# Performance work log

Measured on AMD Instinct MI355X. Metric: run time of the kernel, lower is better.

The kernel has to match this reference:

```python
import jax, jax.numpy as jnp
import numpy as np

DIM = 192
HEADS = 6
HIDDEN = 384  # int(DIM * 2.0)


def _ln(x, w, b):
    # WithBias LayerNorm over channel dim (torch normalizes last dim of b,(hw),c)
    mu = jnp.mean(x, axis=1, keepdims=True)
    var = jnp.var(x, axis=1, keepdims=True)
    return (x - mu) / jnp.sqrt(var + 1e-5) * w[None, :, None, None] + b[None, :, None, None]


def _conv1x1(x, w):  # w: [O, I, 1, 1]
    return jnp.einsum('bihw,oi->bohw', x, w[:, :, 0, 0])


def _dwconv3(x, w):  # depthwise 3x3, w: [C, 1, 3, 3]
    return jax.lax.conv_general_dilated(
        x, w, window_strides=(1, 1), padding=((1, 1), (1, 1)),
        feature_group_count=x.shape[1],
        dimension_numbers=('NCHW', 'OIHW', 'NCHW'))


def _l2norm(x):  # F.normalize along last axis
    n = jnp.sqrt(jnp.sum(x * x, axis=-1, keepdims=True))
    return x / jnp.maximum(n, 1e-12)


def setup_inputs() -> dict:
    key = jax.random.key(0)
    ks = jax.random.split(key, 16)
    s = 0.02
    d = {}
    d['x'] = jax.random.normal(ks[0], (2, DIM, 128, 128), dtype=jnp.float32)
    d['k_v'] = jax.random.normal(ks[1], (2, 256), dtype=jnp.float32)
    d['ln1_w'] = jnp.ones((DIM,), jnp.float32)
    d['ln1_b'] = jnp.zeros((DIM,), jnp.float32)
    d['temp'] = jnp.ones((HEADS, 1, 1), jnp.float32)
    d['w_kR'] = jax.random.normal(ks[2], (DIM * 3 // 4, 192), jnp.float32) * s
    d['w_kI'] = jax.random.normal(ks[3], (DIM // 4, 64), jnp.float32) * s
    d['w_qR'] = jax.random.normal(ks[4], (DIM, DIM * 3 // 4, 1, 1), jnp.float32) * s
    d['w_qdw'] = jax.random.normal(ks[5], (DIM, 1, 3, 3), jnp.float32) * s
    d['w_kvI'] = jax.random.normal(ks[6], (DIM * 2, DIM // 4, 1, 1), jnp.float32) * s
    d['w_kvdw'] = jax.random.normal(ks[7], (DIM * 2, 1, 3, 3), jnp.float32) * s
    d['w_po'] = jax.random.normal(ks[8], (DIM, DIM, 1, 1), jnp.float32) * s
    d['ln2_w'] = jnp.ones((DIM,), jnp.float32)
    d['ln2_b'] = jnp.zeros((DIM,), jnp.float32)
    d['w_ffk'] = jax.random.normal(ks[9], (DIM, 256), jnp.float32) * s
    d['w_pin'] = jax.random.normal(ks[10], (HIDDEN * 2, DIM, 1, 1), jnp.float32) * s
    d['w_dw'] = jax.random.normal(ks[11], (HIDDEN * 2, 1, 3, 3), jnp.float32) * s
    d['w_pout'] = jax.random.normal(ks[12], (DIM, HIDDEN, 1, 1), jnp.float32) * s
    return d


def reference(x, k_v, ln1_w, ln1_b, temp, w_kR, w_kI, w_qR, w_qdw, w_kvI, w_kvdw,
              w_po, ln2_w, ln2_b, w_ffk, w_pin, w_dw, w_pout):
    b, c, h, w = x.shape
    c3 = c * 3 // 4
    # ---- Rttention on norm1(x) ----
    xn = _ln(x, ln1_w, ln1_b)
    kvr = (k_v[:, :192] @ w_kR.T)[:, :, None, None]   # [b, 3c/4, 1, 1]
    kvi = (k_v[:, 192:] @ w_kI.T)[:, :, None, None]   # [b, c/4, 1, 1]
    x_r = xn[:, :c3] * kvr + xn[:, :c3]
    x_i = xn[:, c3:] * kvi + xn[:, c3:]
    q = _dwconv3(_conv1x1(x_r, w_qR), w_qdw)          # [b, c, h, w]
    kv = _dwconv3(_conv1x1(x_i, w_kvI), w_kvdw)       # [b, 2c, h, w]
    k, v = jnp.split(kv, 2, axis=1)
    rh = lambda t: t.reshape(b, HEADS, c // HEADS, h * w)
    q = _l2norm(rh(q))
    k = _l2norm(rh(k))
    v = rh(v)
    # channel-wise attention: [b, head, c_h, c_h]
    attn = jax.nn.softmax(jnp.einsum('bhcd,bhed->bhce', q, k) * temp[None], axis=-1)
    out = jnp.einsum('bhce,bhed->bhcd', attn, v).reshape(b, c, h, w)
    x = x + _conv1x1(out, w_po)
    # ---- GDFN FeedForward on norm2(x) ----
    xn2 = _ln(x, ln2_w, ln2_b)
    kvf = (k_v @ w_ffk.T)[:, :, None, None]           # [b, c, 1, 1]
    y = xn2 * kvf + xn2
    y = _dwconv3(_conv1x1(y, w_pin), w_dw)            # [b, 2*hidden, h, w]
    y1, y2 = jnp.split(y, 2, axis=1)
    y = jax.nn.gelu(y1, approximate=False) * y2
    x = x + _conv1x1(y, w_pout)
    return (x, k_v)
```

## Files before the change

### kernel.cpp

```cpp
#include <hip/hip_runtime.h>
#include <math.h>

#define HW 16384
#define CDIM 192
#define C3 144
#define C4 48
#define NB 2
#define NPX 32768
#define HEADS 6

typedef unsigned short u16;
typedef unsigned int u32;
typedef __attribute__((ext_vector_type(8))) short bf16x8;
typedef __attribute__((ext_vector_type(4))) float f32x4;

__device__ __forceinline__ float bf2f(u16 u) {
    return __uint_as_float(((unsigned int)u) << 16);
}
__device__ __forceinline__ u16 f2bf(float f) {
    unsigned int x = __float_as_uint(f);
    unsigned int r = x + 0x7fffu + ((x >> 16) & 1u);
    return (u16)(r >> 16);
}

static inline float* wsf(void* ws, size_t off) { return (float*)((char*)ws + off); }
static inline u16* wsh(void* ws, size_t off) { return (u16*)((char*)ws + off); }

__global__ void k_setup(const float* __restrict__ kvv, const float* __restrict__ wkR,
                        const float* __restrict__ wkI, const float* __restrict__ wffk,
                        const float* __restrict__ wqR, const float* __restrict__ wkvI,
                        const float* __restrict__ wpo, const float* __restrict__ wpin,
                        const float* __restrict__ wpout,
                        const float* __restrict__ ln2w, const float* __restrict__ ln2b,
                        u16* __restrict__ wb, float* __restrict__ sm,
                        float* __restrict__ A2, float* __restrict__ B2,
                        float* __restrict__ tail) {
    int t = blockIdx.x * 256 + threadIdx.x;
    if (t < 313344) {
        float v;
        if (t < 30720) {
            int o = t / 160, i = t % 160;
            v = (i < 144) ? wqR[o * 144 + i] : 0.f;
        } else if (t < 55296) {
            int r = t - 30720; int o = r / 64, i = r % 64;
            v = (i < 48) ? wkvI[o * 48 + i] : 0.f;
        } else if (t < 92160) {
            v = wpo[t - 55296];
        } else if (t < 239616) {
            v = wpin[t - 92160];
        } else {
            v = wpout[t - 239616];
        }
        wb[t] = f2bf(v);
    } else if (t < 314112) {
        int r = t - 313344;
        if (r < 288) {
            int b = r / 144, o = r % 144;
            const float* v = kvv + b * 256;
            const float* w = wkR + o * 192;
            float s = 0.f;
            for (int j = 0; j < 192; j++) s += v[j] * w[j];
            sm[r] = s + 1.0f;
        } else if (r < 384) {
            int r2 = r - 288;
            int b = r2 / 48, o = r2 % 48;
            const float* v = kvv + b * 256 + 192;
            const float* w = wkI + o * 64;
            float s = 0.f;
            for (int j = 0; j < 64; j++) s += v[j] * w[j];
            sm[288 + r2] = s + 1.0f;
        } else {
            int r2 = r - 384;
            int b = r2 / 192, o = r2 % 192;
            const float* v = kvv + b * 256;
            const float* w = wffk + o * 256;
            float s = 0.f;
            for (int j = 0; j < 256; j++) s += v[j] * w[j];
            float sc = s + 1.0f;
            sm[384 + r2] = sc;
            A2[r2] = ln2w[o] * sc;
            B2[r2] = ln2b[o] * sc;
        }
    } else if (t < 314624) {
        int r = t - 314112;
        tail[r] = kvv[r];
    }
}

__global__ __launch_bounds__(256) void k_ln1(
    const float* __restrict__ xin,
    const float* __restrict__ lnw, const float* __restrict__ lnb,
    const float* __restrict__ sca, const float* __restrict__ scb,
    u16* __restrict__ outA, u16* __restrict__ outB) {
    __shared__ float red[2][16][16][4];
    __shared__ float mu_s[16][4], rstd_s[16][4];
    int t = threadIdx.x;
    int px4 = t & 15, cg = t >> 4;
    int base = blockIdx.x * 64;
    int b = base >> 14;
    int p = (base & 16383) + px4 * 4;
    float vals[12][4];
    float s[4] = {0.f, 0.f, 0.f, 0.f}, s2[4] = {0.f, 0.f, 0.f, 0.f};
#pragma unroll
    for (int j = 0; j < 12; j++) {
        int c = cg * 12 + j;
        size_t off = ((size_t)(b * CDIM + c)) * HW + p;
        float4 f = *(const float4*)(xin + off);
        float v[4] = {f.x, f.y, f.z, f.w};
#pragma unroll
        for (int q = 0; q < 4; q++) {
            vals[j][q] = v[q]; s[q] += v[q]; s2[q] += v[q] * v[q];
        }
    }
#pragma unroll
    for (int q = 0; q < 4; q++) { red[0][cg][px4][q] = s[q]; red[1][cg][px4][q] = s2[q]; }
    __syncthreads();
    if (t < 16) {
        float S[4] = {0.f, 0.f, 0.f, 0.f}, S2[4] = {0.f, 0.f, 0.f, 0.f};
        for (int g2 = 0; g2 < 16; g2++)
#pragma unroll
            for (int q = 0; q < 4; q++) { S[q] += red[0][g2][t][q]; S2[q] += red[1][g2][t][q]; }
#pragma unroll
        for (int q = 0; q < 4; q++) {
            float mu = S[q] * (1.0f / CDIM);
            float var = S2[q] * (1.0f / CDIM) - mu * mu;
            mu_s[t][q] = mu;
            rstd_s[t][q] = rsqrtf(var + 1e-5f);
        }
    }
    __syncthreads();
    float mu[4], rs[4];
#pragma unroll
    for (int q = 0; q < 4; q++) { mu[q] = mu_s[px4][q]; rs[q] = rstd_s[px4][q]; }
    float Ac[12], Bc[12];
#pragma unroll
    for (int j = 0; j < 12; j++) {
        int c = cg * 12 + j;
        float sc = (c < C3) ? sca[b * C3 + c] : scb[b * C4 + (c - C3)];
        Ac[j] = lnw[c] * sc;
        Bc[j] = lnb[c] * sc;
    }
    int isR = (cg < 12);
    size_t row0 = (size_t)b * HW + p;
    u16* basep = isR ? (outA + row0 * 160 + cg * 12)
                     : (outB + row0 * 64 + (cg * 12 - 144));
    int rowlen = isR ? 160 : 64;
#pragma unroll
    for (int q = 0; q < 4; q++) {
        u16 tmp[12];
#pragma unroll
        for (int j = 0; j < 12; j++)
            tmp[j] = f2bf((vals[j][q] - mu[q]) * rs[q] * Ac[j] + Bc[j]);
        u16* op = basep + q * rowlen;
        ushort4 o0 = {tmp[0], tmp[1], tmp[2], tmp[3]};
        ushort4 o1 = {tmp[4], tmp[5], tmp[6], tmp[7]};
        ushort4 o2 = {tmp[8], tmp[9], tmp[10], tmp[11]};
        *(ushort4*)(op) = o0;
        *(ushort4*)(op + 4) = o1;
        *(ushort4*)(op + 8) = o2;
    }
    if (cg == 0) {
        int4 z = {0, 0, 0, 0};
#pragma unroll
        for (int q = 0; q < 4; q++) {
            u16* pr = outA + (row0 + q) * 160 + 144;
            *(int4*)(pr) = z; *(int4*)(pr + 8) = z;
            u16* pi = outB + (row0 + q) * 64 + 48;
            *(int4*)(pi) = z; *(int4*)(pi + 8) = z;
        }
    }
}

template <int NCH, int MLOOP, int MODE>
__global__ __launch_bounds__(256, 2) void k_gemm_t(
    const u16* __restrict__ X, const u16* __restrict__ Wb,
    const void* __restrict__ resid, void* __restrict__ outp, int CO) {
    constexpr int CIP = NCH * 32;
    const int tid = threadIdx.x;
    const int n0 = blockIdx.x * 128;
    const int b = blockIdx.z;
    const int wave = tid >> 6, lane = tid & 63;
    const int quad = lane >> 4, l16 = lane & 15;
    const u16* brow = X + ((size_t)b * HW + n0 + wave * 32 + l16) * CIP + quad * 8;
    bf16x8 Bf[NCH][2];
#pragma unroll
    for (int ch = 0; ch < NCH; ch++) {
        Bf[ch][0] = *(const bf16x8*)(brow + ch * 32);
        Bf[ch][1] = *(const bf16x8*)(brow + 16 * CIP + ch * 32);
    }
#pragma unroll
    for (int ml = 0; ml < MLOOP; ml++) {
        const int m0 = (blockIdx.y * MLOOP + ml) * 64;
        const u16* arow = Wb + (size_t)(m0 + l16) * CIP + quad * 8;
        f32x4 acc[4][2] = {};
#pragma unroll
        for (int ch = 0; ch < NCH; ch++) {
            bf16x8 af[4];
#pragma unroll
            for (int mi = 0; mi < 4; mi++)
                af[mi] = *(const bf16x8*)(arow + mi * 16 * CIP + ch * 32);
#pragma unroll
            for (int mi = 0; mi < 4; mi++) {
                acc[mi][0] = __builtin_amdgcn_mfma_f32_16x16x32_bf16(af[mi], Bf[ch][0], acc[mi][0], 0, 0, 0);
                acc[mi][1] = __builtin_amdgcn_mfma_f32_16x16x32_bf16(af[mi], Bf[ch][1], acc[mi][1], 0, 0, 0);
            }
        }
#pragma unroll
        for (int mi = 0; mi < 4; mi++) {
#pragma unroll
            for (int ni = 0; ni < 2; ni++) {
                int c0 = m0 + mi * 16 + quad * 4;
                int px = n0 + wave * 32 + ni * 16 + l16;
                if (MODE == 0) {
                    u16* ob = (u16*)outp + ((size_t)b * CO + c0) * HW + px;
#pragma unroll
                    for (int r = 0; r < 4; r++) ob[(size_t)r * HW] = f2bf(acc[mi][ni][r]);
                } else {
                    const float* rp = (const float*)resid + ((size_t)b * 192 + c0) * HW + px;
                    ushort4 o;
                    o.x = f2bf(acc[mi][ni][0] + rp[0]);
                    o.y = f2bf(acc[mi][ni][1] + rp[(size_t)HW]);
                    o.z = f2bf(acc[mi][ni][2] + rp[(size_t)2 * HW]);
                    o.w = f2bf(acc[mi][ni][3] + rp[(size_t)3 * HW]);
                    *(ushort4*)((u16*)outp + ((size_t)b * HW + px) * 192 + c0) = o;
                }
            }
        }
    }
}

__global__ __launch_bounds__(256) void k_gemm_s(
    const u16* __restrict__ X, const u16* __restrict__ Wb,
    const u16* __restrict__ residT, float* __restrict__ outp) {
    constexpr int NCH = 12;
    constexpr int CIP = NCH * 32;
    __shared__ __align__(16) u16 Ws[64 * 32];
    __shared__ __align__(16) u16 Xs[32 * 130];
    const int tid = threadIdx.x;
    const int n0 = blockIdx.x * 128;
    const int m0 = blockIdx.y * 64;
    const int b = blockIdx.z;
    const u16* Xb = X + (size_t)b * 384 * HW + n0;
    const int wave = tid >> 6, lane = tid & 63;
    const int quad = lane >> 4, l16 = lane & 15;
    const int smr = tid >> 2, sk4 = tid & 3;
    const int skr = tid >> 3, sc0 = (tid & 7) * 16;
    f32x4 acc[4][2] = {};
    for (int ch = 0; ch < NCH; ch++) {
        const int k0 = ch * 32;
        if (ch) __syncthreads();
        {
            const int4 wv = *(const int4*)(Wb + (size_t)(m0 + smr) * CIP + k0 + sk4 * 8);
            *(int4*)&Ws[(smr << 5) + (((sk4 ^ (smr & 3)) & 3) << 3)] = wv;
        }
        {
            const u16* xc = Xb + (size_t)(k0 + skr) * HW + sc0;
            int4 r0 = *(const int4*)xc;
            int4 r1 = *(const int4*)(xc + 8);
            u32* dst = (u32*)&Xs[skr * 130 + sc0];
#pragma unroll
            for (int i = 0; i < 4; i++) dst[i] = ((const u32*)&r0)[i];
#pragma unroll
            for (int i = 0; i < 4; i++) dst[4 + i] = ((const u32*)&r1)[i];
        }
        __syncthreads();
        bf16x8 af[4];
#pragma unroll
        for (int mi = 0; mi < 4; mi++) {
            int row = mi * 16 + l16;
            af[mi] = *(const bf16x8*)&Ws[(row << 5) + ((quad ^ (row & 3)) << 3)];
        }
#pragma unroll
        for (int ni = 0; ni < 2; ni++) {
            int n = wave * 32 + ni * 16 + l16;
            bf16x8 bfr;
#pragma unroll
            for (int j = 0; j < 8; j++) bfr[j] = (short)Xs[(quad * 8 + j) * 130 + n];
#pragma unroll
            for (int mi = 0; mi < 4; mi++)
                acc[mi][ni] = __builtin_amdgcn_mfma_f32_16x16x32_bf16(af[mi], bfr, acc[mi][ni], 0, 0, 0);
        }
    }
#pragma unroll
    for (int mi = 0; mi < 4; mi++) {
#pragma unroll
        for (int ni = 0; ni < 2; ni++) {
            int c0 = m0 + mi * 16 + quad * 4;
            int px = n0 + wave * 32 + ni * 16 + l16;
            ushort4 rv = *(const ushort4*)(residT + ((size_t)b * HW + px) * 192 + c0);
            float* ob = outp + ((size_t)b * 192 + c0) * HW + px;
            ob[0] = acc[mi][ni][0] + bf2f(rv.x);
            ob[(size_t)HW] = acc[mi][ni][1] + bf2f(rv.y);
            ob[(size_t)2 * HW] = acc[mi][ni][2] + bf2f(rv.z);
            ob[(size_t)3 * HW] = acc[mi][ni][3] + bf2f(rv.w);
        }
    }
}

__global__ __launch_bounds__(256) void k_dw2(const u16* __restrict__ X,
                                             const float* __restrict__ Wd,
                                             u16* __restrict__ out, int C, int sqCh,
                                             float* __restrict__ sqp) {
    __shared__ float In[34 * 132];
    __shared__ float red[4];
    int bc = blockIdx.x >> 2, rt = blockIdx.x & 3;
    int b = bc / C, ch = bc % C;
    const u16* xb = X + (size_t)bc * HW;
    int t = threadIdx.x;
    int c0 = (t & 7) * 16;
    for (int r = t >> 3; r < 34; r += 32) {
        int y = rt * 32 - 1 + r;
        float* dst = &In[r * 132 + 1 + c0];
        if ((unsigned)y < 128u) {
            const u16* src = xb + y * 128 + c0;
            int4 r0 = *(const int4*)src;
            int4 r1 = *(const int4*)(src + 8);
            const u16* p0 = (const u16*)&r0;
            const u16* p1 = (const u16*)&r1;
#pragma unroll
            for (int i = 0; i < 8; i++) dst[i] = bf2f(p0[i]);
#pragma unroll
            for (int i = 0; i < 8; i++) dst[8 + i] = bf2f(p1[i]);
        } else {
#pragma unroll
            for (int i = 0; i < 16; i++) dst[i] = 0.f;
        }
    }
    if (t < 34) { In[t * 132] = 0.f; In[t * 132 + 129] = 0.f; }
    __syncthreads();
    const float* w = Wd + ch * 9;
    float w00 = w[0], w01 = w[1], w02 = w[2], w10 = w[3], w11 = w[4],
          w12 = w[5], w20 = w[6], w21 = w[7], w22 = w[8];
    int x = t & 127, rg = t >> 7;
    int base = rg * 16;
    float A2 = 0.f, A1 = 0.f, B1 = 0.f, ssq = 0.f;
    u16* ob = out + (size_t)bc * HW + (rt * 32 + base) * 128 + x;
#pragma unroll
    for (int r = 0; r < 18; r++) {
        const float* row = &In[(base + r) * 132 + x];
        float v0 = row[0], v1 = row[1], v2 = row[2];
        float h0 = w00 * v0 + w01 * v1 + w02 * v2;
        float h1 = w10 * v0 + w11 * v1 + w12 * v2;
        float h2 = w20 * v0 + w21 * v1 + w22 * v2;
        if (r >= 2) {
            float val = A2 + B1 + h2;
            ob[(size_t)(r - 2) * 128] = f2bf(val);
            ssq += val * val;
        }
        A2 = A1; A1 = h0; B1 = h1;
    }
    if (ch < sqCh) {
        for (int o = 32; o > 0; o >>= 1) ssq += __shfl_down(ssq, o, 64);
        int wid = t >> 6, lane = t & 63;
        if (lane == 0) red[wid] = ssq;
        __syncthreads();
        if (t == 0) sqp[((b * 192 + ch) << 2) | rt] = red[0] + red[1] + red[2] + red[3];
    }
}

__global__ __launch_bounds__(256) void k_dw_gelu2(const u16* __restrict__ G0,
                                                  const float* __restrict__ Wd,
                                                  u16* __restrict__ out) {
    __shared__ float In[2 * 34 * 132];
    int bc = blockIdx.x >> 2, rt = blockIdx.x & 3;
    int b = bc / 384, j = bc % 384;
    int t = threadIdx.x;
    int c0 = (t & 7) * 16;
    for (int pl = 0; pl < 2; pl++) {
        const u16* xb = G0 + ((size_t)b * 768 + pl * 384 + j) * HW;
        float* pla = &In[pl * 34 * 132];
        for (int r = t >> 3; r < 34; r += 32) {
            int y = rt * 32 - 1 + r;
            float* dst = &pla[r * 132 + 1 + c0];
            if ((unsigned)y < 128u) {
                const u16* src = xb + y * 128 + c0;
                int4 r0 = *(const int4*)src;
                int4 r1 = *(const int4*)(src + 8);
                const u16* p0 = (const u16*)&r0;
                const u16* p1 = (const u16*)&r1;
#pragma unroll
                for (int i = 0; i < 8; i++) dst[i] = bf2f(p0[i]);
#pragma unroll
                for (int i = 0; i < 8; i++) dst[8 + i] = bf2f(p1[i]);
            } else {
#pragma unroll
                for (int i = 0; i < 16; i++) dst[i] = 0.f;
            }
        }
        if (t < 34) { pla[t * 132] = 0.f; pla[t * 132 + 129] = 0.f; }
    }
    __syncthreads();
    const float* w1 = Wd + j * 9;
    const float* w2 = Wd + (384 + j) * 9;
    float a00 = w1[0], a01 = w1[1], a02 = w1[2], a10 = w1[3], a11 = w1[4],
          a12 = w1[5], a20 = w1[6], a21 = w1[7], a22 = w1[8];
    float b00 = w2[0], b01 = w2[1], b02 = w2[2], b10 = w2[3], b11 = w2[4],
          b12 = w2[5], b20 = w2[6], b21 = w2[7], b22 = w2[8];
    int x = t & 127, rg = t >> 7;
    int base = rg * 16;
    float A2a = 0.f, A1a = 0.f, B1a = 0.f;
    float A2b = 0.f, A1b = 0.f, B1b = 0.f;
    u16* ob = out + ((size_t)b * 384 + j) * HW + (rt * 32 + base) * 128 + x;
#pragma unroll
    for (int r = 0; r < 18; r++) {
        const float* r1p = &In[(base + r) * 132 + x];
        const float* r2p = r1p + 34 * 132;
        float u0 = r1p[0], u1 = r1p[1], u2 = r1p[2];
        float v0 = r2p[0], v1 = r2p[1], v2 = r2p[2];
        float h0a = a00 * u0 + a01 * u1 + a02 * u2;
        float h1a = a10 * u0 + a11 * u1 + a12 * u2;
        float h2a = a20 * u0 + a21 * u1 + a22 * u2;
        float h0b = b00 * v0 + b01 * v1 + b02 * v2;
        float h1b = b10 * v0 + b11 * v1 + b12 * v2;
        float h2b = b20 * v0 + b21 * v1 + b22 * v2;
        if (r >= 2) {
            float s1 = A2a + B1a + h2a;
            float s2 = A2b + B1b + h2b;
            float g = 0.5f * s1 * (1.0f + erff(s1 * 0.70710678118654752f));
            ob[(size_t)(r - 2) * 128] = f2bf(g * s2);
        }
        A2a = A1a; A1a = h0a; B1a = h1a;
        A2b = A1b; A1b = h0b; B1b = h1b;
    }
}

__global__ __launch_bounds__(256) void k_qk(const u16* __restrict__ qb_,
                                            const u16* __restrict__ kb_,
                                            float* __restrict__ Spart) {
    int bh = blockIdx.x >> 6, ds = blockIdx.x & 63;
    int b = bh / HEADS, h = bh % HEADS;
    int tid = threadIdx.x;
    int wave = tid >> 6, lane = tid & 63;
    int quad = lane >> 4, l16 = lane & 15;
    int tm = wave >> 1, tn = wave & 1;
    const u16* qrow = qb_ + ((size_t)(b * 192 + h * 32 + tm * 16 + l16)) * HW + ds * 256 + quad * 8;
    const u16* krow = kb_ + ((size_t)(b * 384 + h * 32 + tn * 16 + l16)) * HW + ds * 256 + quad * 8;
    f32x4 acc = {};
    bf16x8 qa[3], ka[3];
    auto ld = [&](int s, int cc) {
        qa[s] = *(const bf16x8*)(qrow + cc * 32);
        ka[s] = *(const bf16x8*)(krow + cc * 32);
    };
    ld(0, 0); ld(1, 1);
#pragma unroll
    for (int ch = 0; ch < 8; ch++) {
        if (ch + 2 < 8) ld((ch + 2) % 3, ch + 2);
        acc = __builtin_amdgcn_mfma_f32_16x16x32_bf16(qa[ch % 3], ka[ch % 3], acc, 0, 0, 0);
    }
    float* Sb = Spart + ((size_t)ds * 12 + bh) * 1024;
#pragma unroll
    for (int r = 0; r < 4; r++)
        Sb[(tm * 16 + quad * 4 + r) * 32 + tn * 16 + l16] = acc[r];
}

__global__ void k_softmax(const float* __restrict__ Spart, const float* __restrict__ sqqp,
                          const float* __restrict__ sqkp, const float* __restrict__ temp,
                          u16* __restrict__ attnb) {
    int row = blockIdx.x;
    int bh = row >> 5, c2 = row & 31;
    int b = bh / HEADS, h = bh % HEADS;
    int e = threadIdx.x;
    float l = -1e30f;
    if (e < 32) {
        float s = 0.f;
        for (int d = 0; d < 64; d++) s += Spart[((size_t)d * 12 + bh) * 1024 + c2 * 32 + e];
        const float* qp = sqqp + (b * 192 + h * 32 + c2) * 4;
        const float* kp = sqkp + (b * 192 + h * 32 + e) * 4;
        float nq = qp[0] + qp[1] + qp[2] + qp[3];
        float nk = kp[0] + kp[1] + kp[2] + kp[3];
        float invq = 1.0f / fmaxf(sqrtf(nq), 1e-12f);
        float invk = 1.0f / fmaxf(sqrtf(nk), 1e-12f);
        l = s * invq * invk * temp[h];
    }
    float m = l;
    for (int o = 32; o > 0; o >>= 1) m = fmaxf(m, __shfl_xor(m, o, 64));
    float ev = (e < 32) ? expf(l - m) : 0.f;
    float ssum = ev;
    for (int o = 32; o > 0; o >>= 1) ssum += __shfl_xor(ssum, o, 64);
    if (e < 32) attnb[bh * 1024 + c2 * 32 + e] = f2bf(ev / ssum);
}

__global__ __launch_bounds__(256) void k_av(const u16* __restrict__ attnb,
                                            const u16* __restrict__ kvb,
                                            u16* __restrict__ out) {
    __shared__ __align__(16) u16 Vs[32 * 130];
    int bh = blockIdx.x >> 7;
    int pt = blockIdx.x & 127;
    int b = bh / HEADS, h = bh % HEADS;
    int p0 = pt * 128;
    int t = threadIdx.x;
    {
        int e = t >> 3, c0 = (t & 7) * 16;
        const u16* src = kvb + ((size_t)(b * 384 + 192 + h * 32 + e)) * HW + p0 + c0;
        int4 r0 = *(const int4*)src;
        int4 r1 = *(const int4*)(src + 8);
        u32* dst = (u32*)&Vs[e * 130 + c0];
#pragma unroll
        for (int i = 0; i < 4; i++) dst[i] = ((const u32*)&r0)[i];
#pragma unroll
        for (int i = 0; i < 4; i++) dst[4 + i] = ((const u32*)&r1)[i];
    }
    __syncthreads();
    int wave = t >> 6, lane = t & 63;
    int quad = lane >> 4, l16 = lane & 15;
    f32x4 acc[2][2] = {};
    bf16x8 af[2];
#pragma unroll
    for (int tm = 0; tm < 2; tm++)
        af[tm] = *(const bf16x8*)(attnb + bh * 1024 + (tm * 16 + l16) * 32 + quad * 8);
#pragma unroll
    for (int nt = 0; nt < 2; nt++) {
        int n = wave * 32 + nt * 16 + l16;
        bf16x8 bfr;
#pragma unroll
        for (int j = 0; j < 8; j++) bfr[j] = (short)Vs[(quad * 8 + j) * 130 + n];
#pragma unroll
        for (int tm = 0; tm < 2; tm++)
            acc[tm][nt] = __builtin_amdgcn_mfma_f32_16x16x32_bf16(af[tm], bfr, acc[tm][nt], 0, 0, 0);
    }
#pragma unroll
    for (int tm = 0; tm < 2; tm++)
#pragma unroll
        for (int nt = 0; nt < 2; nt++) {
            int c0 = h * 32 + tm * 16 + quad * 4;
            int px = p0 + wave * 32 + nt * 16 + l16;
            ushort4 o;
            o.x = f2bf(acc[tm][nt][0]);
            o.y = f2bf(acc[tm][nt][1]);
            o.z = f2bf(acc[tm][nt][2]);
            o.w = f2bf(acc[tm][nt][3]);
            *(ushort4*)(out + ((size_t)b * HW + px) * 192 + c0) = o;
        }
}

__global__ __launch_bounds__(256) void k_ln2t(
    const u16* __restrict__ xin, const float* __restrict__ A2,
    const float* __restrict__ B2, u16* __restrict__ outp) {
    int t = threadIdx.x;
    int pxg = blockIdx.x * 64 + (t >> 2);
    int l2 = t & 3;
    int b = pxg >> 14;
    const u16* src = xin + (size_t)pxg * 192 + l2 * 48;
    float v[48];
    float s = 0.f, s2 = 0.f;
#pragma unroll
    for (int i = 0; i < 6; i++) {
        int4 r0 = *(const int4*)(src + i * 8);
        const u16* pp = (const u16*)&r0;
#pragma unroll
        for (int k = 0; k < 8; k++) {
            float f = bf2f(pp[k]);
            v[i * 8 + k] = f; s += f; s2 += f * f;
        }
    }
    s += __shfl_xor(s, 1, 64);  s += __shfl_xor(s, 2, 64);
    s2 += __shfl_xor(s2, 1, 64); s2 += __shfl_xor(s2, 2, 64);
    float mu = s * (1.0f / CDIM);
    float rstd = rsqrtf(s2 * (1.0f / CDIM) - mu * mu + 1e-5f);
    const float* Ap = A2 + b * 192 + l2 * 48;
    const float* Bp = B2 + b * 192 + l2 * 48;
    u16* dst = outp + (size_t)pxg * 192 + l2 * 48;
#pragma unroll
    for (int i = 0; i < 12; i++) {
        float4 a = *(const float4*)(Ap + i * 4);
        float4 bb = *(const float4*)(Bp + i * 4);
        ushort4 o;
        o.x = f2bf((v[i * 4 + 0] - mu) * rstd * a.x + bb.x);
        o.y = f2bf((v[i * 4 + 1] - mu) * rstd * a.y + bb.y);
        o.z = f2bf((v[i * 4 + 2] - mu) * rstd * a.z + bb.z);
        o.w = f2bf((v[i * 4 + 3] - mu) * rstd * a.w + bb.w);
        *(ushort4*)(dst + i * 4) = o;
    }
}

extern "C" void kernel_launch(void* const* d_in, const int* in_sizes, int n_in,
                              void* d_out, int out_size, void* d_ws, size_t ws_size,
                              hipStream_t stream) {
    const float* x     = (const float*)d_in[0];
    const float* k_v   = (const float*)d_in[1];
    const float* ln1w  = (const float*)d_in[2];
    const float* ln1b  = (const float*)d_in[3];
    const float* temp  = (const float*)d_in[4];
    const float* w_kR  = (const float*)d_in[5];
    const float* w_kI  = (const float*)d_in[6];
    const float* w_qR  = (const float*)d_in[7];
    const float* w_qdw = (const float*)d_in[8];
    const float* w_kvI = (const float*)d_in[9];
    const float* w_kvdw= (const float*)d_in[10];
    const float* w_po  = (const float*)d_in[11];
    const float* ln2w  = (const float*)d_in[12];
    const float* ln2b  = (const float*)d_in[13];
    const float* w_ffk = (const float*)d_in[14];
    const float* w_pin = (const float*)d_in[15];
    const float* w_dw  = (const float*)d_in[16];
    const float* w_pout= (const float*)d_in[17];
    float* out = (float*)d_out;

    const size_t MiB = 1048576ULL;
    u16*   q0b     = wsh(d_ws, 0);
    u16*   attnoutb= wsh(d_ws, 0);
    u16*   y0b     = wsh(d_ws, 0);
    u16*   kv0b    = wsh(d_ws, 12 * MiB);
    u16*   ybufb   = wsh(d_ws, 12 * MiB);
    u16*   x1b     = wsh(d_ws, 36 * MiB);
    u16*   qbuf_b  = wsh(d_ws, 48 * MiB);
    u16*   kvbuf_b = wsh(d_ws, 60 * MiB);
    u16*   xrb     = wsh(d_ws, 84 * MiB);
    u16*   xib     = wsh(d_ws, 94 * MiB);
    u16*   g0b     = wsh(d_ws, 98 * MiB);
    u16*   wb      = wsh(d_ws, 146 * MiB);
    float* sm      = wsf(d_ws, 147 * MiB);
    float* Spart   = wsf(d_ws, 0);
    u16* wq   = wb;
    u16* wkv  = wb + 30720;
    u16* wpo  = wb + 55296;
    u16* wpin = wb + 92160;
    u16* wpout= wb + 239616;
    float* kvr  = sm;
    float* kvi  = sm + 288;
    float* sqqp = sm + 768;
    float* sqkp = sm + 2304;
    u16*   attnb= (u16*)(sm + 3840);
    float* A2c  = sm + 10240;
    float* B2c  = sm + 10624;

    k_setup<<<1229, 256, 0, stream>>>(k_v, w_kR, w_kI, w_ffk, w_qR, w_kvI, w_po,
                                      w_pin, w_pout, ln2w, ln2b, wb, sm, A2c, B2c,
                                      out + (size_t)NB * CDIM * HW);
    k_ln1<<<NPX / 64, 256, 0, stream>>>(x, ln1w, ln1b, kvr, kvi, xrb, xib);
    k_gemm_t<5, 3, 0><<<dim3(128, 1, 2), 256, 0, stream>>>(xrb, wq, nullptr, q0b, 192);
    k_gemm_t<2, 3, 0><<<dim3(128, 2, 2), 256, 0, stream>>>(xib, wkv, nullptr, kv0b, 384);
    k_dw2<<<NB * 192 * 4, 256, 0, stream>>>(q0b, w_qdw, qbuf_b, 192, 192, sqqp);
    k_dw2<<<NB * 384 * 4, 256, 0, stream>>>(kv0b, w_kvdw, kvbuf_b, 384, 192, sqkp);
    k_qk<<<12 * 64, 256, 0, stream>>>(qbuf_b, kvbuf_b, Spart);
    k_softmax<<<384, 64, 0, stream>>>(Spart, sqqp, sqkp, temp, attnb);
    k_av<<<12 * 128, 256, 0, stream>>>(attnb, kvbuf_b, attnoutb);
    k_gemm_t<6, 3, 1><<<dim3(128, 1, 2), 256, 0, stream>>>(attnoutb, wpo, x, x1b, 192);
    k_ln2t<<<NPX / 64, 256, 0, stream>>>(x1b, A2c, B2c, y0b);
    k_gemm_t<6, 6, 0><<<dim3(128, 2, 2), 256, 0, stream>>>(y0b, wpin, nullptr, g0b, 768);
    k_dw_gelu2<<<NB * 384 * 4, 256, 0, stream>>>(g0b, w_dw, ybufb);
    k_gemm_s<<<dim3(128, 3, 2), 256, 0, stream>>>(ybufb, wpout, x1b, out);
}
```

Measured before the change: 297.7 us.

## Split GEMM M-loop into separate blocks with XCD-aware block remapping

```diff
diff --git a/kernel.cpp b/kernel.cpp
--- a/kernel.cpp
+++ b/kernel.cpp
@@ -171,59 +171,59 @@
     }
 }
 
-template <int NCH, int MLOOP, int MODE>
-__global__ __launch_bounds__(256, 2) void k_gemm_t(
+template <int NCH, int MT, int MODE>
+__global__ __launch_bounds__(256) void k_gemm_t(
     const u16* __restrict__ X, const u16* __restrict__ Wb,
     const void* __restrict__ resid, void* __restrict__ outp, int CO) {
     constexpr int CIP = NCH * 32;
+    const int bid = blockIdx.x;
+    const int q8 = gridDim.x >> 3;
+    const int l = (bid & 7) * q8 + (bid >> 3);
+    const int b = l / (128 * MT);
+    const int r = l % (128 * MT);
+    const int xc = r / (MT * 16);
+    const int r2 = r % (MT * 16);
+    const int m0 = (r2 >> 4) * 64;
+    const int n0 = (xc * 16 + (r2 & 15)) * 128;
     const int tid = threadIdx.x;
-    const int n0 = blockIdx.x * 128;
-    const int b = blockIdx.z;
     const int wave = tid >> 6, lane = tid & 63;
     const int quad = lane >> 4, l16 = lane & 15;
+    const u16* arow = Wb + (size_t)(m0 + l16) * CIP + quad * 8;
     const u16* brow = X + ((size_t)b * HW + n0 + wave * 32 + l16) * CIP + quad * 8;
-    bf16x8 Bf[NCH][2];
+    f32x4 acc[4][2] = {};
 #pragma unroll
     for (int ch = 0; ch < NCH; ch++) {
-        Bf[ch][0] = *(const bf16x8*)(brow + ch * 32);
-        Bf[ch][1] = *(const bf16x8*)(brow + 16 * CIP + ch * 32);
-    }
-#pragma unroll
-    for (int ml = 0; ml < MLOOP; ml++) {
-        const int m0 = (blockIdx.y * MLOOP + ml) * 64;
-        const u16* arow = Wb + (size_t)(m0 + l16) * CIP + quad * 8;
-        f32x4 acc[4][2] = {};
-#pragma unroll
-        for (int ch = 0; ch < NCH; ch++) {
-            bf16x8 af[4];
-#pragma unroll
-            for (int mi = 0; mi < 4; mi++)
-                af[mi] = *(const bf16x8*)(arow + mi * 16 * CIP + ch * 32);
-#pragma unroll
-            for (int mi = 0; mi < 4; mi++) {
-                acc[mi][0] = __builtin_amdgcn_mfma_f32_16x16x32_bf16(af[mi], Bf[ch][0], acc[mi][0], 0, 0, 0);
-                acc[mi][1] = __builtin_amdgcn_mfma_f32_16x16x32_bf16(af[mi], Bf[ch][1], acc[mi][1], 0, 0, 0);
-            }
-        }
+        const int k0 = ch * 32;
+        bf16x8 bf0 = *(const bf16x8*)(brow + k0);
+        bf16x8 bf1 = *(const bf16x8*)(brow + 16 * CIP + k0);
+        bf16x8 af[4];
+#pragma unroll
+        for (int mi = 0; mi < 4; mi++)
+            af[mi] = *(const bf16x8*)(arow + mi * 16 * CIP + k0);
 #pragma unroll
         for (int mi = 0; mi < 4; mi++) {
-#pragma unroll
-            for (int ni = 0; ni < 2; ni++) {
-                int c0 = m0 + mi * 16 + quad * 4;
-                int px = n0 + wave * 32 + ni * 16 + l16;
-                if (MODE == 0) {
-                    u16* ob = (u16*)outp + ((size_t)b * CO + c0) * HW + px;
-#pragma unroll
-                    for (int r = 0; r < 4; r++) ob[(size_t)r * HW] = f2bf(acc[mi][ni][r]);
-                } else {
-                    const float* rp = (const float*)resid + ((size_t)b * 192 + c0) * HW + px;
-                    ushort4 o;
-                    o.x = f2bf(acc[mi][ni][0] + rp[0]);
-                    o.y = f2bf(acc[mi][ni][1] + rp[(size_t)HW]);
-                    o.z = f2bf(acc[mi][ni][2] + rp[(size_t)2 * HW]);
-                    o.w = f2bf(acc[mi][ni][3] + rp[(size_t)3 * HW]);
-                    *(ushort4*)((u16*)outp + ((size_t)b * HW + px) * 192 + c0) = o;
-                }
+            acc[mi][0] = __builtin_amdgcn_mfma_f32_16x16x32_bf16(af[mi], bf0, acc[mi][0], 0, 0, 0);
+            acc[mi][1] = __builtin_amdgcn_mfma_f32_16x16x32_bf16(af[mi], bf1, acc[mi][1], 0, 0, 0);
+        }
+    }
+#pragma unroll
+    for (int mi = 0; mi < 4; mi++) {
+#pragma unroll
+        for (int ni = 0; ni < 2; ni++) {
+            int c0 = m0 + mi * 16 + quad * 4;
+            int px = n0 + wave * 32 + ni * 16 + l16;
+            if (MODE == 0) {
+                u16* ob = (u16*)outp + ((size_t)b * CO + c0) * HW + px;
+#pragma unroll
+                for (int rr = 0; rr < 4; rr++) ob[(size_t)rr * HW] = f2bf(acc[mi][ni][rr]);
+            } else {
+                const float* rp = (const float*)resid + ((size_t)b * 192 + c0) * HW + px;
+                ushort4 o;
+                o.x = f2bf(acc[mi][ni][0] + rp[0]);
+                o.y = f2bf(acc[mi][ni][1] + rp[(size_t)HW]);
+                o.z = f2bf(acc[mi][ni][2] + rp[(size_t)2 * HW]);
+                o.w = f2bf(acc[mi][ni][3] + rp[(size_t)3 * HW]);
+                *(ushort4*)((u16*)outp + ((size_t)b * HW + px) * 192 + c0) = o;
             }
         }
     }
@@ -628,16 +628,16 @@
                                       w_pin, w_pout, ln2w, ln2b, wb, sm, A2c, B2c,
                                       out + (size_t)NB * CDIM * HW);
     k_ln1<<<NPX / 64, 256, 0, stream>>>(x, ln1w, ln1b, kvr, kvi, xrb, xib);
-    k_gemm_t<5, 3, 0><<<dim3(128, 1, 2), 256, 0, stream>>>(xrb, wq, nullptr, q0b, 192);
-    k_gemm_t<2, 3, 0><<<dim3(128, 2, 2), 256, 0, stream>>>(xib, wkv, nullptr, kv0b, 384);
+    k_gemm_t<5, 3, 0><<<NB * 128 * 3, 256, 0, stream>>>(xrb, wq, nullptr, q0b, 192);
+    k_gemm_t<2, 6, 0><<<NB * 128 * 6, 256, 0, stream>>>(xib, wkv, nullptr, kv0b, 384);
     k_dw2<<<NB * 192 * 4, 256, 0, stream>>>(q0b, w_qdw, qbuf_b, 192, 192, sqqp);
     k_dw2<<<NB * 384 * 4, 256, 0, stream>>>(kv0b, w_kvdw, kvbuf_b, 384, 192, sqkp);
     k_qk<<<12 * 64, 256, 0, stream>>>(qbuf_b, kvbuf_b, Spart);
     k_softmax<<<384, 64, 0, stream>>>(Spart, sqqp, sqkp, temp, attnb);
     k_av<<<12 * 128, 256, 0, stream>>>(attnb, kvbuf_b, attnoutb);
-    k_gemm_t<6, 3, 1><<<dim3(128, 1, 2), 256, 0, stream>>>(attnoutb, wpo, x, x1b, 192);
+    k_gemm_t<6, 3, 1><<<NB * 128 * 3, 256, 0, stream>>>(attnoutb, wpo, x, x1b, 192);
     k_ln2t<<<NPX / 64, 256, 0, stream>>>(x1b, A2c, B2c, y0b);
-    k_gemm_t<6, 6, 0><<<dim3(128, 2, 2), 256, 0, stream>>>(y0b, wpin, nullptr, g0b, 768);
+    k_gemm_t<6, 12, 0><<<NB * 128 * 12, 256, 0, stream>>>(y0b, wpin, nullptr, g0b, 768);
     k_dw_gelu2<<<NB * 384 * 4, 256, 0, stream>>>(g0b, w_dw, ybufb);
     k_gemm_s<<<dim3(128, 3, 2), 256, 0, stream>>>(ybufb, wpout, x1b, out);
 }
```

After: 311.7 us. 4.7% more time.
